# Kernel tuning notes

Measured on AMD Instinct MI355X. Metric: run time of the kernel, lower is better.

## Reference

```python
import jax, jax.numpy as jnp
import numpy as np

N = 50000
E = 800000
D = 128   # input_dim
O = 128   # output_dim


def setup_inputs() -> dict:
    key = jax.random.key(0)
    ks = jax.random.split(key, 12)
    s = 0.05
    inp = {
        "x": jax.random.normal(ks[0], (N, D), dtype=jnp.float32),
        "edge_index": jax.random.randint(ks[1], (2, E), 0, N, dtype=jnp.int64),
        # lin_src_to_dst / lin_dst_to_src
        "w_s2d": jax.random.normal(ks[2], (D, O), dtype=jnp.float32) * s,
        "b_s2d": jnp.zeros((O,), dtype=jnp.float32),
        "w_d2s": jax.random.normal(ks[3], (D, O), dtype=jnp.float32) * s,
        "b_d2s": jnp.zeros((O,), dtype=jnp.float32),
        # edge_mlp: Linear(2D -> D), ReLU, Linear(D -> 1)
        "w_e1": jax.random.normal(ks[4], (2 * D, D), dtype=jnp.float32) * s,
        "b_e1": jnp.zeros((D,), dtype=jnp.float32),
        "w_e2": jax.random.normal(ks[5], (D, 1), dtype=jnp.float32) * s,
        "b_e2": jnp.zeros((1,), dtype=jnp.float32),
        # gate_mlp: Linear(2O -> O), ReLU, Linear(O -> 1)
        "w_g1": jax.random.normal(ks[6], (2 * O, O), dtype=jnp.float32) * s,
        "b_g1": jnp.zeros((O,), dtype=jnp.float32),
        "w_g2": jax.random.normal(ks[7], (O, 1), dtype=jnp.float32) * s,
        "b_g2": jnp.zeros((1,), dtype=jnp.float32),
    }
    return inp


def reference(x, edge_index, w_s2d, b_s2d, w_d2s, b_d2s,
              w_e1, b_e1, w_e2, b_e2, w_g1, b_g1, w_g2, b_g2):
    num_nodes = x.shape[0]
    src = edge_index[0]
    dst = edge_index[1]

    x_src = x[src]                      # [E, D]
    x_dst = x[dst]                      # [E, D]

    # edge-wise contribution score a_ij in (0,1)
    edge_input = jnp.concatenate([x_src, x_dst], axis=-1)          # [E, 2D]
    h_e = jax.nn.relu(edge_input @ w_e1 + b_e1)                    # [E, D]
    edge_score = jax.nn.sigmoid((h_e @ w_e2 + b_e2)[:, 0])         # [E]

    # directional messages, scaled by edge score
    msg_in = (x_src @ w_s2d + b_s2d) * edge_score[:, None]         # [E, O]
    msg_out = (x_dst @ w_d2s + b_d2s) * edge_score[:, None]        # [E, O]

    # scatter-add to nodes
    h_in = jax.ops.segment_sum(msg_in, dst, num_segments=num_nodes)   # [N, O]
    h_out = jax.ops.segment_sum(msg_out, src, num_segments=num_nodes) # [N, O]

    # degree normalization (clamped at 1)
    ones = jnp.ones((src.shape[0],), dtype=x.dtype)
    in_deg = jnp.maximum(jax.ops.segment_sum(ones, dst, num_segments=num_nodes), 1.0)
    out_deg = jnp.maximum(jax.ops.segment_sum(ones, src, num_segments=num_nodes), 1.0)
    h_in = h_in / in_deg[:, None]
    h_out = h_out / out_deg[:, None]

    # node-wise gate fusing the two directions
    gate_input = jnp.concatenate([h_in, h_out], axis=-1)           # [N, 2O]
    h_g = jax.nn.relu(gate_input @ w_g1 + b_g1)                    # [N, O]
    g = jax.nn.sigmoid(h_g @ w_g2 + b_g2)                          # [N, 1]

    fused = g * h_in + (1.0 - g) * h_out                           # [N, O]
    # input_dim == output_dim -> residual is Identity
    return fused + x
```

## Files before the change

### kernel.cpp

```cpp
#include <hip/hip_runtime.h>

#define N_NODES 50000
#define N_EDGES 800000
#define NBKT 391
#define BKT 128
#define MAXREC 2560
#define EPB 4096
#define XCBLK 6250
#define CNTBLK 196

typedef unsigned int u32;
typedef unsigned short u16;
typedef __attribute__((ext_vector_type(2))) float float2v;
typedef __attribute__((ext_vector_type(8))) short bf16x8;
typedef __attribute__((ext_vector_type(4))) float f32x4;

__device__ __forceinline__ float bf_lo(u32 v){ return __uint_as_float(v << 16); }
__device__ __forceinline__ float bf_hi(u32 v){ return __uint_as_float(v & 0xffff0000u); }
__device__ __forceinline__ u16 f2bf(float f){
    u32 u = __float_as_uint(f);
    u += 0x7fffu + ((u >> 16) & 1u);
    return (u16)(u >> 16);
}

#if __has_builtin(__builtin_amdgcn_cvt_pk_f32_fp8) && __has_builtin(__builtin_amdgcn_cvt_pk_fp8_f32)
#define HW_FP8 1
#else
#define HW_FP8 0
#endif

__device__ __forceinline__ u32 enc1_e4m3(float f){
    u32 u = __float_as_uint(f);
    u32 s = (u >> 24) & 0x80u;
    u32 a = u & 0x7fffffffu;
    if (a >= 0x43e00000u) return s | 0x7eu;
    if (a < 0x3c800000u){
        float af = __uint_as_float(a) * 512.f;
        u32 m = (u32)(af + 0.5f);
        return s | m;
    }
    int e = (int)(a >> 23) - 127;
    u32 mant = (a >> 20) & 7u;
    u32 rnd = (a >> 19) & 1u;
    u32 sticky = (a & 0x7ffffu) ? 1u : 0u;
    u32 code = ((u32)(e + 7) << 3) | mant;
    code += (rnd & (sticky | (mant & 1u)));
    if (code > 0x7eu) code = 0x7eu;
    return s | code;
}

template<bool HI>
__device__ __forceinline__ float2v dec2_word(u32 v){
#if HW_FP8
    return __builtin_amdgcn_cvt_pk_f32_fp8(v, HI);
#else
    u32 v16 = HI ? (v >> 16) : (v & 0xffffu);
    float2v r;
    #pragma unroll
    for (int t = 0; t < 2; t++){
        u32 b = (v16 >> (8 * t)) & 0xffu;
        u32 e = (b >> 3) & 15u, m = b & 7u;
        float fv = e ? __uint_as_float(((e + 120u) << 23) | (m << 20)) : (float)m * 0.001953125f;
        r[t] = (b & 0x80u) ? -fv : fv;
    }
    return r;
#endif
}
__device__ __forceinline__ u32 encpk_lo(float a, float b, u32 old){
#if HW_FP8
    return (u32)__builtin_amdgcn_cvt_pk_fp8_f32(a, b, (int)old, false);
#else
    return (old & 0xffff0000u) | enc1_e4m3(a) | (enc1_e4m3(b) << 8);
#endif
}
__device__ __forceinline__ u32 encpk_hi(float a, float b, u32 old){
#if HW_FP8
    return (u32)__builtin_amdgcn_cvt_pk_fp8_f32(a, b, (int)old, true);
#else
    return (old & 0x0000ffffu) | (enc1_e4m3(a) << 16) | (enc1_e4m3(b) << 24);
#endif
}

__global__ __launch_bounds__(256) void setup_kernel(const float* __restrict__ x,
        const float* __restrict__ w_s2d, const float* __restrict__ w_d2s,
        const float* __restrict__ w_e1, const float* __restrict__ w_g1,
        const float* __restrict__ b_e1, const int* __restrict__ eidx,
        uint2* __restrict__ xb2, u32* __restrict__ xf8,
        u16* __restrict__ pk1, u16* __restrict__ pkM,
        u16* __restrict__ pkG, float* __restrict__ bias1,
        u32* __restrict__ bcnt, u32* __restrict__ bhist){
    const int blk = blockIdx.x, tid = threadIdx.x;
    if (blk < XCBLK){
        int i = blk * 256 + tid;
        float4 v = ((const float4*)x)[i];
        uint2 o;
        o.x = (u32)f2bf(v.x) | ((u32)f2bf(v.y) << 16);
        o.y = (u32)f2bf(v.z) | ((u32)f2bf(v.w) << 16);
        xb2[i] = o;
        u32 w8 = encpk_lo(v.x, v.y, 0u);
        xf8[i] = encpk_hi(v.z, v.w, w8);
    } else if (blk < XCBLK + 386){
        int idx = (blk - XCBLK) * 256 + tid;
        if (idx < 32768){
            int j = idx & 7, g = (idx >> 3) & 3, ch = (idx >> 5) & 255, ks = idx >> 13;
            int k = ks * 32 + g * 8 + j;
            float v = (ch < 128) ? w_e1[k * 128 + ch] : w_e1[(128 + k) * 128 + (ch - 128)];
            pk1[idx] = f2bf(v);
        } else if (idx < 65536){
            int i2 = idx - 32768;
            int j = i2 & 7, g = (i2 >> 3) & 3, ch = (i2 >> 5) & 255, ks = i2 >> 13;
            int k = ks * 32 + g * 8 + j;
            float v = (ch < 128) ? w_s2d[k * 128 + ch] : w_d2s[k * 128 + (ch - 128)];
            pkM[i2] = f2bf(v);
        } else if (idx < 98304){
            int i2 = idx - 65536;
            int j = i2 & 7, g = (i2 >> 3) & 3, oc = (i2 >> 5) & 127, ks = i2 >> 12;
            int k = ks * 32 + g * 8 + j;
            pkG[i2] = f2bf(w_g1[k * 128 + oc]);
        } else if (idx < 98560){
            int o = idx - 98304;
            bias1[o] = (o < 128) ? b_e1[o] : 0.f;
        }
    } else {
        __shared__ u32 h[2 * NBKT];
        const int cb = blk - XCBLK - 386;
        for (int i = tid; i < 2 * NBKT; i += 256) h[i] = 0u;
        __syncthreads();
        const int e0 = cb * EPB;
        for (int i = tid; i < EPB; i += 256){
            int e = e0 + i;
            if (e < N_EDGES){
                atomicAdd(&h[eidx[N_EDGES + e] >> 7], 1u);
                atomicAdd(&h[NBKT + (eidx[e] >> 7)], 1u);
            }
        }
        __syncthreads();
        for (int i = tid; i < 2 * NBKT; i += 256){
            u32 v = h[i];
            bhist[cb * 2 * NBKT + i] = v;
            if (v) atomicAdd(&bcnt[i], v);
        }
    }
}

__global__ __launch_bounds__(256) void proj_mfma_kernel(const u16* __restrict__ xb16,
        const u16* __restrict__ pk1, const float* __restrict__ bias1, u32* __restrict__ T1){
    const int tid = threadIdx.x;
    const int w = tid >> 6, l = tid & 63;
    const int l16 = l & 15, lg = l >> 4;
    const int n0 = blockIdx.x * 16;
    const int node = n0 + l16;
    bf16x8 bx[4];
    #pragma unroll
    for (int ks = 0; ks < 4; ks++)
        bx[ks] = *(const bf16x8*)(xb16 + node * 128 + ks * 32 + lg * 8);
    #pragma unroll
    for (int ct = 0; ct < 4; ct++){
        const int ch0 = w * 64 + ct * 16;
        f32x4 acc = {0.f, 0.f, 0.f, 0.f};
        #pragma unroll
        for (int ks = 0; ks < 4; ks++){
            bf16x8 a = *(const bf16x8*)(pk1 + ((ks * 256 + ch0 + l16) * 4 + lg) * 8);
            acc = __builtin_amdgcn_mfma_f32_16x16x32_bf16(a, bx[ks], acc, 0, 0, 0);
        }
        const int chb = ch0 + lg * 4;
        float f0 = acc[0] + bias1[chb],     f1 = acc[1] + bias1[chb + 1];
        float f2 = acc[2] + bias1[chb + 2], f3 = acc[3] + bias1[chb + 3];
        u32 wd = encpk_lo(f0, f1, 0u);
        wd = encpk_hi(f2, f3, wd);
        T1[node * 64 + (chb >> 2)] = wd;
    }
}

__global__ __launch_bounds__(256) void edge_score_kernel(const u32* __restrict__ T1w, const int* __restrict__ eidx,
        const float* __restrict__ w_e2, const float* __restrict__ b_e2,
        u16* __restrict__ score){
    const int l8 = threadIdx.x & 7;
    const int e = blockIdx.x * 32 + (threadIdx.x >> 3);
    const int src = eidx[e];
    const int dst = eidx[N_EDGES + e];
    const uint4 a8 = *(const uint4*)(T1w + src * 64 + l8 * 4);
    const uint4 b8 = *(const uint4*)(T1w + dst * 64 + 32 + l8 * 4);
    const float2v* wv = (const float2v*)(w_e2 + l8 * 16);
    const float2v zero = {0.f, 0.f};
    float2v acc = {0.f, 0.f};
    float2v t;
    t = __builtin_elementwise_max(dec2_word<false>(a8.x) + dec2_word<false>(b8.x), zero); acc += t * wv[0];
    t = __builtin_elementwise_max(dec2_word<true >(a8.x) + dec2_word<true >(b8.x), zero); acc += t * wv[1];
    t = __builtin_elementwise_max(dec2_word<false>(a8.y) + dec2_word<false>(b8.y), zero); acc += t * wv[2];
    t = __builtin_elementwise_max(dec2_word<true >(a8.y) + dec2_word<true >(b8.y), zero); acc += t * wv[3];
    t = __builtin_elementwise_max(dec2_word<false>(a8.z) + dec2_word<false>(b8.z), zero); acc += t * wv[4];
    t = __builtin_elementwise_max(dec2_word<true >(a8.z) + dec2_word<true >(b8.z), zero); acc += t * wv[5];
    t = __builtin_elementwise_max(dec2_word<false>(a8.w) + dec2_word<false>(b8.w), zero); acc += t * wv[6];
    t = __builtin_elementwise_max(dec2_word<true >(a8.w) + dec2_word<true >(b8.w), zero); acc += t * wv[7];
    float p = acc[0] + acc[1];
    p += __shfl_xor(p, 1, 64);
    p += __shfl_xor(p, 2, 64);
    p += __shfl_xor(p, 4, 64);
    if (l8 == 0){
        float sc = 1.f / (1.f + __expf(-(p + b_e2[0])));
        score[e] = f2bf(sc);
    }
}

__global__ __launch_bounds__(512) void bucket_scan_kernel(const u32* __restrict__ bcnt,
        const u32* __restrict__ bhist, u32* __restrict__ bbase, u32* __restrict__ rb){
    __shared__ u32 sa[512], sb[512];
    const int t = threadIdx.x;
    const int side = blockIdx.x;
    const u32* c = bcnt + side * NBKT;
    u32* base = bbase + side * (NBKT + 1);
    sa[t] = (t < NBKT) ? c[t] : 0u;
    __syncthreads();
    u32 *a = sa, *b = sb;
    for (int off = 1; off < 512; off <<= 1){
        u32 v = a[t]; if (t >= off) v += a[t - off];
        b[t] = v; __syncthreads();
        u32* tmp = a; a = b; b = tmp;
    }
    u32 ex = 0;
    if (t < NBKT){
        ex = t ? a[t - 1] : 0u;
        base[t] = ex;
        if (t == NBKT - 1) base[NBKT] = a[t];
    }
    if (t < NBKT){
        u32 run = ex;
        const int col = side * NBKT + t;
        for (int cb = 0; cb < CNTBLK; cb++){
            u32 hv = bhist[cb * 2 * NBKT + col];
            rb[cb * 2 * NBKT + col] = run;
            run += hv;
        }
    }
}

__global__ __launch_bounds__(256) void bucket1_kernel(const int* __restrict__ eidx, const u16* __restrict__ score,
        const u32* __restrict__ rb, uint2* __restrict__ Bd, uint2* __restrict__ Bs){
    __shared__ u32 rbl[2 * NBKT];
    __shared__ u32 ld[NBKT], ls[NBKT];
    const int tid = threadIdx.x;
    for (int i = tid; i < 2 * NBKT; i += 256) rbl[i] = rb[blockIdx.x * 2 * NBKT + i];
    for (int i = tid; i < NBKT; i += 256){ ld[i] = 0u; ls[i] = 0u; }
    __syncthreads();
    const int e0 = blockIdx.x * EPB;
    for (int i = tid; i < EPB; i += 256){
        int e = e0 + i;
        if (e < N_EDGES){
            int src = eidx[e], dst = eidx[N_EDGES + e];
            u32 sc = (u32)score[e] << 16;
            int bd = dst >> 7;
            u32 r = atomicAdd(&ld[bd], 1u);
            Bd[rbl[bd] + r] = make_uint2(sc | (u32)src, (u32)(dst & 127));
            int bs_ = src >> 7;
            u32 r2 = atomicAdd(&ls[bs_], 1u);
            Bs[rbl[NBKT + bs_] + r2] = make_uint2(sc | (u32)dst, (u32)(src & 127));
        }
    }
}

__global__ __launch_bounds__(256) void bucket2_kernel(const uint2* __restrict__ Bd, const uint2* __restrict__ Bs,
        const u32* __restrict__ bbase,
        u32* __restrict__ cnt_dst, u32* __restrict__ start_dst,
        u32* __restrict__ cnt_src, u32* __restrict__ start_src,
        u32* __restrict__ in_pay, u32* __restrict__ out_pay){
    __shared__ u32 pays[MAXREC];
    __shared__ u16 locs[MAXREC];
    __shared__ u32 hist[BKT], nxt[BKT], pref[BKT];
    const int tid = threadIdx.x;
    const int side = blockIdx.x >= NBKT ? 1 : 0;
    const int b = side ? blockIdx.x - NBKT : blockIdx.x;
    const uint2* __restrict__ B = side ? Bs : Bd;
    const u32* bb = bbase + side * (NBKT + 1);
    const u32 base = bb[b];
    const u32 nrec = bb[b + 1] - base;
    u32* cnto = side ? cnt_src : cnt_dst;
    u32* sto  = side ? start_src : start_dst;
    u32* payo = side ? out_pay : in_pay;
    for (int i = tid; i < BKT; i += 256) hist[i] = 0u;
    __syncthreads();
    for (u32 i = tid; i < nrec; i += 256){
        uint2 r = B[base + i];
        if (i < MAXREC){ pays[i] = r.x; locs[i] = (u16)r.y; }
        atomicAdd(&hist[r.y & (BKT - 1)], 1u);
    }
    __syncthreads();
    if (tid < BKT) pref[tid] = hist[tid];
    __syncthreads();
    for (int off = 1; off < BKT; off <<= 1){
        u32 v = 0;
        if (tid < BKT){ v = pref[tid]; if (tid >= off) v += pref[tid - off]; }
        __syncthreads();
        if (tid < BKT) pref[tid] = v;
        __syncthreads();
    }
    if (tid < BKT){
        u32 ex = tid ? pref[tid - 1] : 0u;
        u32 gstart = base + ex;
        nxt[tid] = gstart;
        int node = b * BKT + tid;
        if (node < N_NODES){ cnto[node] = hist[tid]; sto[node] = gstart; }
    }
    __syncthreads();
    for (u32 i = tid; i < nrec; i += 256){
        u32 pay; int loc;
        if (i < MAXREC){ pay = pays[i]; loc = locs[i]; }
        else { uint2 r = B[base + i]; pay = r.x; loc = (int)(r.y & (BKT - 1)); }
        u32 pos = atomicAdd(&nxt[loc], 1u);
        payo[pos] = pay;
    }
}

__global__ __launch_bounds__(256) void gather_kernel(const u32* __restrict__ xf8,
        const u32* __restrict__ in_pay, const u32* __restrict__ out_pay,
        const u32* __restrict__ cnt_dst, const u32* __restrict__ start_dst,
        const u32* __restrict__ cnt_src, const u32* __restrict__ start_src,
        u32* __restrict__ Y, float* __restrict__ ssin, float* __restrict__ ssout){
    const int w = threadIdx.x >> 6, lane = threadIdx.x & 63;
    const int node = blockIdx.x * 2 + (w >> 1);
    const int dir = w & 1;
    const u32* __restrict__ pay = dir ? out_pay : in_pay;
    const u32 deg = dir ? cnt_src[node] : cnt_dst[node];
    const u32 st  = dir ? start_src[node] : start_dst[node];
    const int half = lane >> 5, l5 = lane & 31;
    float2v AL = {0.f, 0.f}, AH = {0.f, 0.f};
    float ss = 0.f;
    u32 j = (u32)half;
    for (; j + 14 < deg; j += 16){
        u32 p0 = pay[st+j],    p1 = pay[st+j+2],  p2 = pay[st+j+4],  p3 = pay[st+j+6];
        u32 p4 = pay[st+j+8],  p5 = pay[st+j+10], p6 = pay[st+j+12], p7 = pay[st+j+14];
        u32 v0 = xf8[(p0 & 0xffffu)*32 + l5], v1 = xf8[(p1 & 0xffffu)*32 + l5];
        u32 v2 = xf8[(p2 & 0xffffu)*32 + l5], v3 = xf8[(p3 & 0xffffu)*32 + l5];
        u32 v4 = xf8[(p4 & 0xffffu)*32 + l5], v5 = xf8[(p5 & 0xffffu)*32 + l5];
        u32 v6 = xf8[(p6 & 0xffffu)*32 + l5], v7 = xf8[(p7 & 0xffffu)*32 + l5];
        float s0 = __uint_as_float(p0 & 0xffff0000u), s1 = __uint_as_float(p1 & 0xffff0000u);
        float s2 = __uint_as_float(p2 & 0xffff0000u), s3 = __uint_as_float(p3 & 0xffff0000u);
        float s4 = __uint_as_float(p4 & 0xffff0000u), s5 = __uint_as_float(p5 & 0xffff0000u);
        float s6 = __uint_as_float(p6 & 0xffff0000u), s7 = __uint_as_float(p7 & 0xffff0000u);
        AL += dec2_word<false>(v0) * s0;  AH += dec2_word<true>(v0) * s0;
        AL += dec2_word<false>(v1) * s1;  AH += dec2_word<true>(v1) * s1;
        AL += dec2_word<false>(v2) * s2;  AH += dec2_word<true>(v2) * s2;
        AL += dec2_word<false>(v3) * s3;  AH += dec2_word<true>(v3) * s3;
        AL += dec2_word<false>(v4) * s4;  AH += dec2_word<true>(v4) * s4;
        AL += dec2_word<false>(v5) * s5;  AH += dec2_word<true>(v5) * s5;
        AL += dec2_word<false>(v6) * s6;  AH += dec2_word<true>(v6) * s6;
        AL += dec2_word<false>(v7) * s7;  AH += dec2_word<true>(v7) * s7;
        ss += s0 + s1 + s2 + s3 + s4 + s5 + s6 + s7;
    }
    for (; j + 6 < deg; j += 8){
        u32 p0 = pay[st+j], p1 = pay[st+j+2], p2 = pay[st+j+4], p3 = pay[st+j+6];
        u32 v0 = xf8[(p0 & 0xffffu)*32 + l5], v1 = xf8[(p1 & 0xffffu)*32 + l5];
        u32 v2 = xf8[(p2 & 0xffffu)*32 + l5], v3 = xf8[(p3 & 0xffffu)*32 + l5];
        float s0 = __uint_as_float(p0 & 0xffff0000u), s1 = __uint_as_float(p1 & 0xffff0000u);
        float s2 = __uint_as_float(p2 & 0xffff0000u), s3 = __uint_as_float(p3 & 0xffff0000u);
        AL += dec2_word<false>(v0) * s0;  AH += dec2_word<true>(v0) * s0;
        AL += dec2_word<false>(v1) * s1;  AH += dec2_word<true>(v1) * s1;
        AL += dec2_word<false>(v2) * s2;  AH += dec2_word<true>(v2) * s2;
        AL += dec2_word<false>(v3) * s3;  AH += dec2_word<true>(v3) * s3;
        ss += s0 + s1 + s2 + s3;
    }
    for (; j < deg; j += 2){
        u32 pl = pay[st + j];
        u32 v = xf8[(pl & 0xffffu)*32 + l5];
        float sc = __uint_as_float(pl & 0xffff0000u);
        AL += dec2_word<false>(v) * sc;
        AH += dec2_word<true>(v) * sc;
        ss += sc;
    }
    float a0 = AL[0], a1 = AL[1], a2 = AH[0], a3 = AH[1];
    a0 += __shfl_xor(a0, 32, 64);
    a1 += __shfl_xor(a1, 32, 64);
    a2 += __shfl_xor(a2, 32, 64);
    a3 += __shfl_xor(a3, 32, 64);
    ss += __shfl_xor(ss, 32, 64);
    if (half == 0){
        uint2 o;
        o.x = (u32)f2bf(a0) | ((u32)f2bf(a1) << 16);
        o.y = (u32)f2bf(a2) | ((u32)f2bf(a3) << 16);
        *(uint2*)(Y + node * 128 + dir * 64 + l5 * 2) = o;
    }
    if (lane == 0){
        if (dir) ssout[node] = ss; else ssin[node] = ss;
    }
}

__global__ __launch_bounds__(256) void finale_mfma_kernel(const u32* __restrict__ Yw,
        const float* __restrict__ x,
        const u16* __restrict__ pkM, const u16* __restrict__ pkG,
        const float* __restrict__ b_s2d, const float* __restrict__ b_d2s,
        const float* __restrict__ ssin, const float* __restrict__ ssout,
        const u32* __restrict__ cnt_dst, const u32* __restrict__ cnt_src,
        const float* __restrict__ b_g1, const float* __restrict__ w_g2, const float* __restrict__ b_g2,
        float* __restrict__ out){
    __shared__ u32 Hsh[16][132];
    __shared__ float part[16][17];
    __shared__ float gl[16];
    const int tid = threadIdx.x;
    const int w = tid >> 6, l = tid & 63;
    const int l16 = l & 15, lg = l >> 4;
    const int n0 = blockIdx.x * 16;
    const int node = n0 + l16;
    const int dir = w >> 1;
    const int cb = (w & 1) * 64;
    const u16* Yh = (const u16*)Yw;
    bf16x8 yf[4];
    #pragma unroll
    for (int ks = 0; ks < 4; ks++)
        yf[ks] = *(const bf16x8*)(Yh + node * 256 + dir * 128 + ks * 32 + lg * 8);
    const float ssv  = dir ? ssout[node] : ssin[node];
    const float dinv = 1.f / fmaxf((float)(dir ? cnt_src[node] : cnt_dst[node]), 1.f);
    const float* bv = dir ? b_d2s : b_s2d;
    #pragma unroll
    for (int ct = 0; ct < 4; ct++){
        const int chl = cb + ct * 16;
        f32x4 acc = {0.f, 0.f, 0.f, 0.f};
        #pragma unroll
        for (int ks = 0; ks < 4; ks++){
            bf16x8 a = *(const bf16x8*)(pkM + ((ks * 256 + dir * 128 + chl + l16) * 4 + lg) * 8);
            acc = __builtin_amdgcn_mfma_f32_16x16x32_bf16(a, yf[ks], acc, 0, 0, 0);
        }
        const int chb = chl + lg * 4;
        float h0 = (acc[0] + ssv * bv[chb])     * dinv;
        float h1 = (acc[1] + ssv * bv[chb + 1]) * dinv;
        float h2 = (acc[2] + ssv * bv[chb + 2]) * dinv;
        float h3 = (acc[3] + ssv * bv[chb + 3]) * dinv;
        const int wi = (dir * 128 + chb) >> 1;
        Hsh[l16][wi]     = (u32)f2bf(h0) | ((u32)f2bf(h1) << 16);
        Hsh[l16][wi + 1] = (u32)f2bf(h2) | ((u32)f2bf(h3) << 16);
    }
    __syncthreads();
    bf16x8 hb[8];
    #pragma unroll
    for (int ks = 0; ks < 8; ks++)
        hb[ks] = *(const bf16x8*)((const u16*)&Hsh[l16][0] + ks * 32 + lg * 8);
    float p = 0.f;
    #pragma unroll
    for (int ct2 = 0; ct2 < 2; ct2++){
        const int oc0 = w * 32 + ct2 * 16;
        f32x4 acc = {0.f, 0.f, 0.f, 0.f};
        #pragma unroll
        for (int ks = 0; ks < 8; ks++){
            bf16x8 a = *(const bf16x8*)(pkG + ((ks * 128 + oc0 + l16) * 4 + lg) * 8);
            acc = __builtin_amdgcn_mfma_f32_16x16x32_bf16(a, hb[ks], acc, 0, 0, 0);
        }
        const int ob = oc0 + lg * 4;
        #pragma unroll
        for (int r = 0; r < 4; r++)
            p += fmaxf(acc[r] + b_g1[ob + r], 0.f) * w_g2[ob + r];
    }
    part[l16][w * 4 + lg] = p;
    __syncthreads();
    if (tid < 16){
        float s = 0.f;
        #pragma unroll
        for (int i = 0; i < 16; i++) s += part[tid][i];
        gl[tid] = 1.f / (1.f + __expf(-(s + b_g2[0])));
    }
    __syncthreads();
    {
        const int nn = tid >> 4, o = (tid & 15) * 8;
        const float gv = gl[nn];
        const int gbase = (n0 + nn) * 128 + o;
        float4 x0 = *(const float4*)(x + gbase);
        float4 x1 = *(const float4*)(x + gbase + 4);
        float r[8];
        #pragma unroll
        for (int t = 0; t < 4; t++){
            u32 hi = Hsh[nn][(o >> 1) + t];
            u32 ho = Hsh[nn][64 + (o >> 1) + t];
            r[2*t]   = gv * bf_lo(hi) + (1.f - gv) * bf_lo(ho);
            r[2*t+1] = gv * bf_hi(hi) + (1.f - gv) * bf_hi(ho);
        }
        *(float4*)(out + gbase)     = make_float4(r[0]+x0.x, r[1]+x0.y, r[2]+x0.z, r[3]+x0.w);
        *(float4*)(out + gbase + 4) = make_float4(r[4]+x1.x, r[5]+x1.y, r[6]+x1.z, r[7]+x1.w);
    }
}

extern "C" void kernel_launch(void* const* d_in, const int* in_sizes, int n_in,
                              void* d_out, int out_size, void* d_ws, size_t ws_size,
                              hipStream_t stream){
    const float* x     = (const float*)d_in[0];
    const int*   ei    = (const int*)d_in[1];
    const float* w_s2d = (const float*)d_in[2];
    const float* b_s2d = (const float*)d_in[3];
    const float* w_d2s = (const float*)d_in[4];
    const float* b_d2s = (const float*)d_in[5];
    const float* w_e1  = (const float*)d_in[6];
    const float* b_e1  = (const float*)d_in[7];
    const float* w_e2  = (const float*)d_in[8];
    const float* b_e2  = (const float*)d_in[9];
    const float* w_g1  = (const float*)d_in[10];
    const float* b_g1  = (const float*)d_in[11];
    const float* w_g2  = (const float*)d_in[12];
    const float* b_g2  = (const float*)d_in[13];
    float* out = (float*)d_out;
    u32*   T1  = (u32*)d_out;
    uint2* Bd  = (uint2*)((u32*)d_out + 3200000);
    uint2* Bs  = Bd + N_EDGES;
    u32*   Y   = (u32*)d_out;

    char* ws = (char*)d_ws;
    size_t off = 0;
    #define TAKE(name, bytes) char* name = ws + off; off += (((size_t)(bytes)) + 511) & ~(size_t)511;
    TAKE(pk1_b,   32768 * 2)
    TAKE(pkM_b,   32768 * 2)
    TAKE(pkG_b,   32768 * 2)
    TAKE(bias1_b, 256 * 4)
    TAKE(xb_b,    (size_t)N_NODES * 128 * 2)
    TAKE(xf8_b,   (size_t)N_NODES * 128)
    TAKE(score_b, (size_t)N_EDGES * 2)
    TAKE(bcnt_b,  (size_t)2 * NBKT * 4)
    TAKE(bbase_b, (size_t)2 * (NBKT + 1) * 4)
    TAKE(bhist_b, (size_t)CNTBLK * 2 * NBKT * 4)
    TAKE(rb_b,    (size_t)CNTBLK * 2 * NBKT * 4)
    TAKE(cnt_b,   (size_t)2 * N_NODES * 4)
    TAKE(sd_b,    (size_t)N_NODES * 4)
    TAKE(ss2_b,   (size_t)N_NODES * 4)
    TAKE(ipay_b,  (size_t)N_EDGES * 4)
    TAKE(opay_b,  (size_t)N_EDGES * 4)
    TAKE(ssin_b,  (size_t)N_NODES * 4)
    TAKE(ssout_b, (size_t)N_NODES * 4)
    #undef TAKE
    (void)ws_size; (void)in_sizes; (void)n_in; (void)out_size;

    hipMemsetAsync(bcnt_b, 0, (size_t)2 * NBKT * 4, stream);
    setup_kernel<<<XCBLK + 386 + CNTBLK, 256, 0, stream>>>(x, w_s2d, w_d2s, w_e1, w_g1, b_e1, ei,
        (uint2*)xb_b, (u32*)xf8_b, (u16*)pk1_b, (u16*)pkM_b, (u16*)pkG_b,
        (float*)bias1_b, (u32*)bcnt_b, (u32*)bhist_b);
    proj_mfma_kernel<<<N_NODES / 16, 256, 0, stream>>>((const u16*)xb_b,
        (const u16*)pk1_b, (const float*)bias1_b, T1);
    edge_score_kernel<<<N_EDGES / 32, 256, 0, stream>>>((const u32*)T1, ei, w_e2, b_e2,
        (u16*)score_b);
    bucket_scan_kernel<<<2, 512, 0, stream>>>((const u32*)bcnt_b, (const u32*)bhist_b,
        (u32*)bbase_b, (u32*)rb_b);
    bucket1_kernel<<<CNTBLK, 256, 0, stream>>>(ei, (const u16*)score_b,
        (const u32*)rb_b, Bd, Bs);
    bucket2_kernel<<<2 * NBKT, 256, 0, stream>>>(Bd, Bs, (const u32*)bbase_b,
        (u32*)cnt_b, (u32*)sd_b, (u32*)cnt_b + N_NODES, (u32*)ss2_b,
        (u32*)ipay_b, (u32*)opay_b);
    gather_kernel<<<N_NODES / 2, 256, 0, stream>>>((const u32*)xf8_b,
        (const u32*)ipay_b, (const u32*)opay_b,
        (const u32*)cnt_b, (const u32*)sd_b, (const u32*)cnt_b + N_NODES, (const u32*)ss2_b,
        Y, (float*)ssin_b, (float*)ssout_b);
    finale_mfma_kernel<<<N_NODES / 16, 256, 0, stream>>>((const u32*)Y, x,
        (const u16*)pkM_b, (const u16*)pkG_b, b_s2d, b_d2s,
        (const float*)ssin_b, (const float*)ssout_b,
        (const u32*)cnt_b, (const u32*)cnt_b + N_NODES,
        b_g1, w_g2, b_g2, out);
}
```

Measured before the change: 218.2 us.

## Fold bucket scan into projection kernel and widen gather to 4 edge groups

The standalone bucket-scan launch is removed. Its work now runs in two extra blocks appended to the MFMA projection kernel, and each of those 256-thread blocks handles two buckets per thread, saving one kernel launch and its serialization gap. The gather kernel now has each lane load 8-byte fp8 chunks (16 lanes per row) and splits edges across 4 lane groups instead of 2, which raises memory-level parallelism per wave. The cost is two extra shuffle-reduction stages, and the serial scan blocks may now become the tail of the projection kernel.

```diff
diff --git a/kernel.cpp b/kernel.cpp
--- a/kernel.cpp
+++ b/kernel.cpp
@@ -8,6 +8,7 @@
 #define EPB 4096
 #define XCBLK 6250
 #define CNTBLK 196
+#define PROJBLK 3125
 
 typedef unsigned int u32;
 typedef unsigned short u16;
@@ -143,32 +144,69 @@
     }
 }
 
-__global__ __launch_bounds__(256) void proj_mfma_kernel(const u16* __restrict__ xb16,
-        const u16* __restrict__ pk1, const float* __restrict__ bias1, u32* __restrict__ T1){
-    const int tid = threadIdx.x;
-    const int w = tid >> 6, l = tid & 63;
-    const int l16 = l & 15, lg = l >> 4;
-    const int n0 = blockIdx.x * 16;
-    const int node = n0 + l16;
-    bf16x8 bx[4];
-    #pragma unroll
-    for (int ks = 0; ks < 4; ks++)
-        bx[ks] = *(const bf16x8*)(xb16 + node * 128 + ks * 32 + lg * 8);
-    #pragma unroll
-    for (int ct = 0; ct < 4; ct++){
-        const int ch0 = w * 64 + ct * 16;
-        f32x4 acc = {0.f, 0.f, 0.f, 0.f};
-        #pragma unroll
-        for (int ks = 0; ks < 4; ks++){
-            bf16x8 a = *(const bf16x8*)(pk1 + ((ks * 256 + ch0 + l16) * 4 + lg) * 8);
-            acc = __builtin_amdgcn_mfma_f32_16x16x32_bf16(a, bx[ks], acc, 0, 0, 0);
-        }
-        const int chb = ch0 + lg * 4;
-        float f0 = acc[0] + bias1[chb],     f1 = acc[1] + bias1[chb + 1];
-        float f2 = acc[2] + bias1[chb + 2], f3 = acc[3] + bias1[chb + 3];
-        u32 wd = encpk_lo(f0, f1, 0u);
-        wd = encpk_hi(f2, f3, wd);
-        T1[node * 64 + (chb >> 2)] = wd;
+__global__ __launch_bounds__(256) void proj_scan_kernel(const u16* __restrict__ xb16,
+        const u16* __restrict__ pk1, const float* __restrict__ bias1, u32* __restrict__ T1,
+        const u32* __restrict__ bcnt, const u32* __restrict__ bhist,
+        u32* __restrict__ bbase, u32* __restrict__ rb){
+    const int blk = blockIdx.x, tid = threadIdx.x;
+    if (blk < PROJBLK){
+        const int w = tid >> 6, l = tid & 63;
+        const int l16 = l & 15, lg = l >> 4;
+        const int node = blk * 16 + l16;
+        bf16x8 bx[4];
+        #pragma unroll
+        for (int ks = 0; ks < 4; ks++)
+            bx[ks] = *(const bf16x8*)(xb16 + node * 128 + ks * 32 + lg * 8);
+        #pragma unroll
+        for (int ct = 0; ct < 4; ct++){
+            const int ch0 = w * 64 + ct * 16;
+            f32x4 acc = {0.f, 0.f, 0.f, 0.f};
+            #pragma unroll
+            for (int ks = 0; ks < 4; ks++){
+                bf16x8 a = *(const bf16x8*)(pk1 + ((ks * 256 + ch0 + l16) * 4 + lg) * 8);
+                acc = __builtin_amdgcn_mfma_f32_16x16x32_bf16(a, bx[ks], acc, 0, 0, 0);
+            }
+            const int chb = ch0 + lg * 4;
+            float f0 = acc[0] + bias1[chb],     f1 = acc[1] + bias1[chb + 1];
+            float f2 = acc[2] + bias1[chb + 2], f3 = acc[3] + bias1[chb + 3];
+            u32 wd = encpk_lo(f0, f1, 0u);
+            wd = encpk_hi(f2, f3, wd);
+            T1[node * 64 + (chb >> 2)] = wd;
+        }
+    } else {
+        __shared__ u32 sa[256], sb[256];
+        const int side = blk - PROJBLK;
+        const u32* c = bcnt + side * NBKT;
+        u32* base = bbase + side * (NBKT + 1);
+        const int t = tid;
+        u32 e0 = (2 * t < NBKT)     ? c[2 * t]     : 0u;
+        u32 e1 = (2 * t + 1 < NBKT) ? c[2 * t + 1] : 0u;
+        sa[t] = e0 + e1;
+        __syncthreads();
+        u32 *a = sa, *b = sb;
+        for (int off2 = 1; off2 < 256; off2 <<= 1){
+            u32 v = a[t]; if (t >= off2) v += a[t - off2];
+            b[t] = v; __syncthreads();
+            u32* tmp = a; a = b; b = tmp;
+        }
+        u32 exp = t ? a[t - 1] : 0u;
+        if (2 * t < NBKT)     base[2 * t]     = exp;
+        if (2 * t + 1 < NBKT) base[2 * t + 1] = exp + e0;
+        if (t == 255) base[NBKT] = a[255];
+        u32 runs[2] = {exp, exp + e0};
+        #pragma unroll
+        for (int q = 0; q < 2; q++){
+            int cl = 2 * t + q;
+            if (cl < NBKT){
+                u32 run = runs[q];
+                const int col = side * NBKT + cl;
+                for (int cb = 0; cb < CNTBLK; cb++){
+                    u32 hv = bhist[cb * 2 * NBKT + col];
+                    rb[cb * 2 * NBKT + col] = run;
+                    run += hv;
+                }
+            }
+        }
     }
 }
 
@@ -203,38 +241,6 @@
     }
 }
 
-__global__ __launch_bounds__(512) void bucket_scan_kernel(const u32* __restrict__ bcnt,
-        const u32* __restrict__ bhist, u32* __restrict__ bbase, u32* __restrict__ rb){
-    __shared__ u32 sa[512], sb[512];
-    const int t = threadIdx.x;
-    const int side = blockIdx.x;
-    const u32* c = bcnt + side * NBKT;
-    u32* base = bbase + side * (NBKT + 1);
-    sa[t] = (t < NBKT) ? c[t] : 0u;
-    __syncthreads();
-    u32 *a = sa, *b = sb;
-    for (int off = 1; off < 512; off <<= 1){
-        u32 v = a[t]; if (t >= off) v += a[t - off];
-        b[t] = v; __syncthreads();
-        u32* tmp = a; a = b; b = tmp;
-    }
-    u32 ex = 0;
-    if (t < NBKT){
-        ex = t ? a[t - 1] : 0u;
-        base[t] = ex;
-        if (t == NBKT - 1) base[NBKT] = a[t];
-    }
-    if (t < NBKT){
-        u32 run = ex;
-        const int col = side * NBKT + t;
-        for (int cb = 0; cb < CNTBLK; cb++){
-            u32 hv = bhist[cb * 2 * NBKT + col];
-            rb[cb * 2 * NBKT + col] = run;
-            run += hv;
-        }
-    }
-}
-
 __global__ __launch_bounds__(256) void bucket1_kernel(const int* __restrict__ eidx, const u16* __restrict__ score,
         const u32* __restrict__ rb, uint2* __restrict__ Bd, uint2* __restrict__ Bs){
     __shared__ u32 rbl[2 * NBKT];
@@ -322,62 +328,49 @@
     const u32* __restrict__ pay = dir ? out_pay : in_pay;
     const u32 deg = dir ? cnt_src[node] : cnt_dst[node];
     const u32 st  = dir ? start_src[node] : start_dst[node];
-    const int half = lane >> 5, l5 = lane & 31;
-    float2v AL = {0.f, 0.f}, AH = {0.f, 0.f};
+    const int l16 = lane & 15, g = lane >> 4;
+    const uint2* __restrict__ xf2 = (const uint2*)xf8;
+    float2v A0 = {0.f,0.f}, A1 = {0.f,0.f}, A2 = {0.f,0.f}, A3 = {0.f,0.f};
     float ss = 0.f;
-    u32 j = (u32)half;
-    for (; j + 14 < deg; j += 16){
-        u32 p0 = pay[st+j],    p1 = pay[st+j+2],  p2 = pay[st+j+4],  p3 = pay[st+j+6];
-        u32 p4 = pay[st+j+8],  p5 = pay[st+j+10], p6 = pay[st+j+12], p7 = pay[st+j+14];
-        u32 v0 = xf8[(p0 & 0xffffu)*32 + l5], v1 = xf8[(p1 & 0xffffu)*32 + l5];
-        u32 v2 = xf8[(p2 & 0xffffu)*32 + l5], v3 = xf8[(p3 & 0xffffu)*32 + l5];
-        u32 v4 = xf8[(p4 & 0xffffu)*32 + l5], v5 = xf8[(p5 & 0xffffu)*32 + l5];
-        u32 v6 = xf8[(p6 & 0xffffu)*32 + l5], v7 = xf8[(p7 & 0xffffu)*32 + l5];
+    const u32 nfull = deg >> 4;
+    u32 j = (u32)g;
+    for (u32 it = 0; it < nfull; ++it, j += 16){
+        u32 p0 = pay[st+j], p1 = pay[st+j+4], p2 = pay[st+j+8], p3 = pay[st+j+12];
+        uint2 v0 = xf2[(p0 & 0xffffu)*16 + l16], v1 = xf2[(p1 & 0xffffu)*16 + l16];
+        uint2 v2 = xf2[(p2 & 0xffffu)*16 + l16], v3 = xf2[(p3 & 0xffffu)*16 + l16];
         float s0 = __uint_as_float(p0 & 0xffff0000u), s1 = __uint_as_float(p1 & 0xffff0000u);
         float s2 = __uint_as_float(p2 & 0xffff0000u), s3 = __uint_as_float(p3 & 0xffff0000u);
-        float s4 = __uint_as_float(p4 & 0xffff0000u), s5 = __uint_as_float(p5 & 0xffff0000u);
-        float s6 = __uint_as_float(p6 & 0xffff0000u), s7 = __uint_as_float(p7 & 0xffff0000u);
-        AL += dec2_word<false>(v0) * s0;  AH += dec2_word<true>(v0) * s0;
-        AL += dec2_word<false>(v1) * s1;  AH += dec2_word<true>(v1) * s1;
-        AL += dec2_word<false>(v2) * s2;  AH += dec2_word<true>(v2) * s2;
-        AL += dec2_word<false>(v3) * s3;  AH += dec2_word<true>(v3) * s3;
-        AL += dec2_word<false>(v4) * s4;  AH += dec2_word<true>(v4) * s4;
-        AL += dec2_word<false>(v5) * s5;  AH += dec2_word<true>(v5) * s5;
-        AL += dec2_word<false>(v6) * s6;  AH += dec2_word<true>(v6) * s6;
-        AL += dec2_word<false>(v7) * s7;  AH += dec2_word<true>(v7) * s7;
-        ss += s0 + s1 + s2 + s3 + s4 + s5 + s6 + s7;
-    }
-    for (; j + 6 < deg; j += 8){
-        u32 p0 = pay[st+j], p1 = pay[st+j+2], p2 = pay[st+j+4], p3 = pay[st+j+6];
-        u32 v0 = xf8[(p0 & 0xffffu)*32 + l5], v1 = xf8[(p1 & 0xffffu)*32 + l5];
-        u32 v2 = xf8[(p2 & 0xffffu)*32 + l5], v3 = xf8[(p3 & 0xffffu)*32 + l5];
-        float s0 = __uint_as_float(p0 & 0xffff0000u), s1 = __uint_as_float(p1 & 0xffff0000u);
-        float s2 = __uint_as_float(p2 & 0xffff0000u), s3 = __uint_as_float(p3 & 0xffff0000u);
-        AL += dec2_word<false>(v0) * s0;  AH += dec2_word<true>(v0) * s0;
-        AL += dec2_word<false>(v1) * s1;  AH += dec2_word<true>(v1) * s1;
-        AL += dec2_word<false>(v2) * s2;  AH += dec2_word<true>(v2) * s2;
-        AL += dec2_word<false>(v3) * s3;  AH += dec2_word<true>(v3) * s3;
+        A0 += dec2_word<false>(v0.x) * s0;  A1 += dec2_word<true>(v0.x) * s0;
+        A2 += dec2_word<false>(v0.y) * s0;  A3 += dec2_word<true>(v0.y) * s0;
+        A0 += dec2_word<false>(v1.x) * s1;  A1 += dec2_word<true>(v1.x) * s1;
+        A2 += dec2_word<false>(v1.y) * s1;  A3 += dec2_word<true>(v1.y) * s1;
+        A0 += dec2_word<false>(v2.x) * s2;  A1 += dec2_word<true>(v2.x) * s2;
+        A2 += dec2_word<false>(v2.y) * s2;  A3 += dec2_word<true>(v2.y) * s2;
+        A0 += dec2_word<false>(v3.x) * s3;  A1 += dec2_word<true>(v3.x) * s3;
+        A2 += dec2_word<false>(v3.y) * s3;  A3 += dec2_word<true>(v3.y) * s3;
         ss += s0 + s1 + s2 + s3;
     }
-    for (; j < deg; j += 2){
+    for (; j < deg; j += 4){
         u32 pl = pay[st + j];
-        u32 v = xf8[(pl & 0xffffu)*32 + l5];
+        uint2 v = xf2[(pl & 0xffffu)*16 + l16];
         float sc = __uint_as_float(pl & 0xffff0000u);
-        AL += dec2_word<false>(v) * sc;
-        AH += dec2_word<true>(v) * sc;
+        A0 += dec2_word<false>(v.x) * sc;  A1 += dec2_word<true>(v.x) * sc;
+        A2 += dec2_word<false>(v.y) * sc;  A3 += dec2_word<true>(v.y) * sc;
         ss += sc;
     }
-    float a0 = AL[0], a1 = AL[1], a2 = AH[0], a3 = AH[1];
-    a0 += __shfl_xor(a0, 32, 64);
-    a1 += __shfl_xor(a1, 32, 64);
-    a2 += __shfl_xor(a2, 32, 64);
-    a3 += __shfl_xor(a3, 32, 64);
+    #define REDUCE2(X) X[0] += __shfl_xor(X[0], 16, 64); X[1] += __shfl_xor(X[1], 16, 64); \
+                       X[0] += __shfl_xor(X[0], 32, 64); X[1] += __shfl_xor(X[1], 32, 64);
+    REDUCE2(A0) REDUCE2(A1) REDUCE2(A2) REDUCE2(A3)
+    #undef REDUCE2
+    ss += __shfl_xor(ss, 16, 64);
     ss += __shfl_xor(ss, 32, 64);
-    if (half == 0){
-        uint2 o;
-        o.x = (u32)f2bf(a0) | ((u32)f2bf(a1) << 16);
-        o.y = (u32)f2bf(a2) | ((u32)f2bf(a3) << 16);
-        *(uint2*)(Y + node * 128 + dir * 64 + l5 * 2) = o;
+    if (g == 0){
+        uint4 o;
+        o.x = (u32)f2bf(A0[0]) | ((u32)f2bf(A0[1]) << 16);
+        o.y = (u32)f2bf(A1[0]) | ((u32)f2bf(A1[1]) << 16);
+        o.z = (u32)f2bf(A2[0]) | ((u32)f2bf(A2[1]) << 16);
+        o.w = (u32)f2bf(A3[0]) | ((u32)f2bf(A3[1]) << 16);
+        *(uint4*)(Y + node * 128 + dir * 64 + l16 * 4) = o;
     }
     if (lane == 0){
         if (dir) ssout[node] = ss; else ssin[node] = ss;
@@ -527,12 +520,11 @@
     setup_kernel<<<XCBLK + 386 + CNTBLK, 256, 0, stream>>>(x, w_s2d, w_d2s, w_e1, w_g1, b_e1, ei,
         (uint2*)xb_b, (u32*)xf8_b, (u16*)pk1_b, (u16*)pkM_b, (u16*)pkG_b,
         (float*)bias1_b, (u32*)bcnt_b, (u32*)bhist_b);
-    proj_mfma_kernel<<<N_NODES / 16, 256, 0, stream>>>((const u16*)xb_b,
-        (const u16*)pk1_b, (const float*)bias1_b, T1);
+    proj_scan_kernel<<<PROJBLK + 2, 256, 0, stream>>>((const u16*)xb_b,
+        (const u16*)pk1_b, (const float*)bias1_b, T1,
+        (const u32*)bcnt_b, (const u32*)bhist_b, (u32*)bbase_b, (u32*)rb_b);
     edge_score_kernel<<<N_EDGES / 32, 256, 0, stream>>>((const u32*)T1, ei, w_e2, b_e2,
         (u16*)score_b);
-    bucket_scan_kernel<<<2, 512, 0, stream>>>((const u32*)bcnt_b, (const u32*)bhist_b,
-        (u32*)bbase_b, (u32*)rb_b);
     bucket1_kernel<<<CNTBLK, 256, 0, stream>>>(ei, (const u16*)score_b,
         (const u32*)rb_b, Bd, Bs);
     bucket2_kernel<<<2 * NBKT, 256, 0, stream>>>(Bd, Bs, (const u32*)bbase_b,
```

Measured after the change: 219.8 us. No clear change (+0.7%).
